# Kernel tuning notes

Measured on AMD Instinct MI355X. Metric: run time of the kernel, lower is better.

The kernel has to match this reference:

```python
import jax, jax.numpy as jnp
import numpy as np

H = 16  # heads
DH = 64  # dim_head
SCALE = DH ** -0.5


def rotate_half(x):
    x1, x2 = jnp.split(x, 2, axis=-1)
    return jnp.concatenate([-x2, x1], axis=-1)


def apply_rope(pos, t):
    # pos: [n, d] broadcast over [b, h, n, d]
    return t * jnp.cos(pos) + rotate_half(t) * jnp.sin(pos)


def setup_inputs() -> dict:
    key = jax.random.key(0)
    ks = jax.random.split(key, 6)
    B, N, D = 4, 2048, 1024
    inner = H * DH
    x = jax.random.normal(ks[0], (B, N, D), dtype=jnp.float32)
    rotary_emb = jax.random.normal(ks[1], (N, DH), dtype=jnp.float32)
    Wq = jax.random.normal(ks[2], (D, inner), dtype=jnp.float32) / np.sqrt(D)
    Wkv = jax.random.normal(ks[3], (D, 2 * inner), dtype=jnp.float32) / np.sqrt(D)
    Wout = jax.random.normal(ks[4], (inner, D), dtype=jnp.float32) / np.sqrt(inner)
    bout = jnp.zeros((D,), dtype=jnp.float32)
    return {"x": x, "rotary_emb": rotary_emb, "Wq": Wq, "Wkv": Wkv, "Wout": Wout, "bout": bout}


def reference(x, rotary_emb, Wq, Wkv, Wout, bout):
    B, N, D = x.shape
    # QKV projections (self-attention: context = x)
    q = x @ Wq                       # [b, n, h*d]
    kv = x @ Wkv                     # [b, n, 2*h*d]
    k, v = jnp.split(kv, 2, axis=-1)

    def to_heads(t):
        return t.reshape(B, N, H, DH).transpose(0, 2, 1, 3)  # [b, h, n, d]

    q, k, v = to_heads(q), to_heads(k), to_heads(v)
    q = apply_rope(rotary_emb, q)
    k = apply_rope(rotary_emb, k)

    # scaled dot-product attention
    scores = jnp.einsum('bhid,bhjd->bhij', q, k) * SCALE
    attn = jax.nn.softmax(scores, axis=-1)
    out = jnp.einsum('bhij,bhjd->bhid', attn, v)  # [b, h, n, d]
    out = out.transpose(0, 2, 1, 3).reshape(B, N, H * DH)
    return out @ Wout + bout
```

## Files before the change

### kernel.cpp

```cpp
#include <hip/hip_runtime.h>

#define BB 4
#define NN 2048
#define DD 1024
#define HH 16
#define DHH 64
#define MM (BB*NN)
#define QS 3072

typedef unsigned short u16;
typedef __attribute__((ext_vector_type(8))) short short8;
typedef __attribute__((ext_vector_type(4))) float floatx4;

#if __has_builtin(__builtin_amdgcn_exp2f)
#define EXP2F __builtin_amdgcn_exp2f
#else
#define EXP2F exp2f
#endif

__device__ __forceinline__ u16 f2bf(float f) {
  union { float f; unsigned u; } v; v.f = f;
  unsigned u = v.u;
  return (u16)((u + 0x7fffu + ((u >> 16) & 1u)) >> 16);
}
__device__ __forceinline__ float bf2f(u16 h) {
  union { unsigned u; float f; } v; v.u = ((unsigned)h) << 16;
  return v.f;
}
__device__ __forceinline__ unsigned fbits(float f) {
  union { float f; unsigned u; } v; v.f = f; return v.u;
}
__device__ __forceinline__ unsigned pkbf(float lo, float hi) {
#if __has_builtin(__builtin_amdgcn_perm)
  return __builtin_amdgcn_perm(fbits(hi), fbits(lo), 0x07060302u);
#else
  return (fbits(lo) >> 16) | (fbits(hi) & 0xffff0000u);
#endif
}
__device__ __forceinline__ void gll16(const u16* g, u16* l) {
  __builtin_amdgcn_global_load_lds((const __attribute__((address_space(1))) unsigned int*)g,
                                   (__attribute__((address_space(3))) unsigned int*)l, 16, 0, 0);
}
__device__ __forceinline__ int toff(int row, int kc) {
  int pr = row >> 1;
  int c = (((row & 1) << 2) + kc) ^ (pr & 7);
  return pr * 64 + c * 8;
}

#define SOFTMAX_SCALE 0.18033688f
#define SOFTMAX_BIAS  -28.8539008f

__global__ __launch_bounds__(256) void cvt_kernel(const float* __restrict__ in,
                                                  u16* __restrict__ out, int n) {
  int i = (blockIdx.x * 256 + threadIdx.x) * 4;
  if (i >= n) return;
  float4 v = *(const float4*)(in + i);
  u16 o[4] = {f2bf(v.x), f2bf(v.y), f2bf(v.z), f2bf(v.w)};
  *(uint2*)(out + i) = *(uint2*)o;
}

__global__ __launch_bounds__(256) void tcvt3_kernel(const float* __restrict__ Wq,
                                                    const float* __restrict__ Wkv,
                                                    const float* __restrict__ Wout,
                                                    u16* __restrict__ WT,
                                                    u16* __restrict__ WoutT) {
  __shared__ float t[64][65];
  int bx = blockIdx.x;
  const float* src;
  u16* dst;
  int C, c0;
  if (bx < 16)      { src = Wq;   dst = WT;                       C = 1024; c0 = bx * 64; }
  else if (bx < 48) { src = Wkv;  dst = WT + (size_t)DD * DD;     C = 2048; c0 = (bx - 16) * 64; }
  else              { src = Wout; dst = WoutT;                    C = 1024; c0 = (bx - 48) * 64; }
  const int R = 1024;
  int r0 = blockIdx.y * 64;
  int tid = threadIdx.x;
#pragma unroll
  for (int i = 0; i < 16; ++i) {
    int lin = i * 256 + tid;
    int rr = lin >> 6, cc = lin & 63;
    t[rr][cc] = src[(size_t)(r0 + rr) * C + c0 + cc];
  }
  __syncthreads();
#pragma unroll
  for (int i = 0; i < 16; ++i) {
    int lin = i * 256 + tid;
    int rr = lin >> 6, cc = lin & 63;
    dst[(size_t)(c0 + rr) * R + r0 + cc] = f2bf(t[cc][rr]);
  }
}

__global__ __launch_bounds__(256) void rope_tab_kernel(const float* __restrict__ rot,
                                                       float2* __restrict__ tab) {
  int i = blockIdx.x * 256 + threadIdx.x;
  float p = rot[i];
  float s, c;
  __sincosf(p, &s, &c);
  tab[i] = make_float2(c, s);
}

__global__ __launch_bounds__(512, 2) void gemm_qkv(const u16* __restrict__ A,
                                                   const u16* __restrict__ Bt,
                                                   u16* __restrict__ qd,
                                                   u16* __restrict__ kd,
                                                   u16* __restrict__ vt,
                                                   const float2* __restrict__ tab) {
  const int K = DD;
  const int NT = K / 64;
  __shared__ __align__(16) u16 lds[65536];
  int tid = threadIdx.x;
  int wave = tid >> 6, lane = tid & 63;
  int q4 = lane >> 4, l16 = lane & 15;
  int wr = wave >> 2, wc = wave & 3;

  int flat = blockIdx.y * 12 + blockIdx.x;
  int wg = (flat & 7) * 48 + (flat >> 3);
  int bx = wg % 12, by = wg / 12;
  int m0 = by * 256, n0 = bx * 256;

  const u16* Ag = A + (size_t)m0 * K;
  const u16* Bg = Bt + (size_t)n0 * K;

  int spr = tid >> 3, sct = tid & 7, su = sct ^ (spr & 7);
  int srow = spr * 2 + (su >> 2);
  int skc = (su & 3) * 8;
  size_t so = (size_t)srow * K + skc;

  int toffA[8], toffB[4];
#pragma unroll
  for (int mi = 0; mi < 8; ++mi) toffA[mi] = wr * 4096 + toff(mi * 16 + l16, q4);
#pragma unroll
  for (int ni = 0; ni < 4; ++ni)
    toffB[ni] = (wc >> 1) * 4096 + toff((wc & 1) * 64 + ni * 16 + l16, q4);

  floatx4 acc[8][4];
#pragma unroll
  for (int mi = 0; mi < 8; ++mi)
#pragma unroll
    for (int ni = 0; ni < 4; ++ni) acc[mi][ni] = (floatx4){0.f, 0.f, 0.f, 0.f};

  auto stageHalf = [&](int t, int mat, int kh) {
    const u16* src = (mat ? Bg : Ag) + so + t * 64 + kh * 32;
    u16* dst = lds + (t & 1) * 32768 + mat * 16384 + kh * 8192 + wave * 512;
    gll16(src, dst);
    gll16(src + (size_t)128 * K, dst + 4096);
  };

  stageHalf(0, 1, 0); stageHalf(0, 0, 0); stageHalf(0, 1, 1); stageHalf(0, 0, 1);
  stageHalf(1, 1, 0); stageHalf(1, 0, 0); stageHalf(1, 1, 1);
  __builtin_amdgcn_s_waitcnt(0x0F76);
  __builtin_amdgcn_s_barrier();

#pragma unroll
  for (int t = 0; t < NT; ++t) {
    const u16* Ab = lds + (t & 1) * 32768;
    const u16* Bb = Ab + 16384;
    short8 af[4], bfq[4];

#pragma unroll
    for (int ni = 0; ni < 4; ++ni) bfq[ni] = *(const short8*)(Bb + toffB[ni]);
#pragma unroll
    for (int f = 0; f < 4; ++f) af[f] = *(const short8*)(Ab + toffA[f]);
    if (t + 1 < NT) stageHalf(t + 1, 0, 1);
    __builtin_amdgcn_s_barrier();
    __builtin_amdgcn_s_waitcnt(0xC07F);
    __builtin_amdgcn_s_setprio(1);
#pragma unroll
    for (int f = 0; f < 4; ++f)
#pragma unroll
      for (int ni = 0; ni < 4; ++ni)
        acc[f][ni] = __builtin_amdgcn_mfma_f32_16x16x32_bf16(af[f], bfq[ni], acc[f][ni], 0, 0, 0);
    __builtin_amdgcn_s_setprio(0);
    __builtin_amdgcn_s_barrier();

#pragma unroll
    for (int f = 0; f < 4; ++f) af[f] = *(const short8*)(Ab + toffA[4 + f]);
    if (t + 2 < NT) stageHalf(t + 2, 1, 0);
    __builtin_amdgcn_s_barrier();
    __builtin_amdgcn_s_waitcnt(0xC07F);
    __builtin_amdgcn_s_setprio(1);
#pragma unroll
    for (int f = 0; f < 4; ++f)
#pragma unroll
      for (int ni = 0; ni < 4; ++ni)
        acc[4 + f][ni] = __builtin_amdgcn_mfma_f32_16x16x32_bf16(af[f], bfq[ni], acc[4 + f][ni], 0, 0, 0);
    __builtin_amdgcn_s_setprio(0);
    __builtin_amdgcn_s_barrier();

#pragma unroll
    for (int ni = 0; ni < 4; ++ni) bfq[ni] = *(const short8*)(Bb + 8192 + toffB[ni]);
#pragma unroll
    for (int f = 0; f < 4; ++f) af[f] = *(const short8*)(Ab + 8192 + toffA[f]);
    if (t + 2 < NT) stageHalf(t + 2, 0, 0);
    __builtin_amdgcn_s_barrier();
    __builtin_amdgcn_s_waitcnt(0xC07F);
    __builtin_amdgcn_s_setprio(1);
#pragma unroll
    for (int f = 0; f < 4; ++f)
#pragma unroll
      for (int ni = 0; ni < 4; ++ni)
        acc[f][ni] = __builtin_amdgcn_mfma_f32_16x16x32_bf16(af[f], bfq[ni], acc[f][ni], 0, 0, 0);
    __builtin_amdgcn_s_setprio(0);
    __builtin_amdgcn_s_barrier();

#pragma unroll
    for (int f = 0; f < 4; ++f) af[f] = *(const short8*)(Ab + 8192 + toffA[4 + f]);
    if (t + 2 < NT) stageHalf(t + 2, 1, 1);
    __builtin_amdgcn_s_barrier();
    __builtin_amdgcn_s_waitcnt(0xC07F);
    __builtin_amdgcn_s_setprio(1);
#pragma unroll
    for (int f = 0; f < 4; ++f)
#pragma unroll
      for (int ni = 0; ni < 4; ++ni)
        acc[4 + f][ni] = __builtin_amdgcn_mfma_f32_16x16x32_bf16(af[f], bfq[ni], acc[4 + f][ni], 0, 0, 0);
    __builtin_amdgcn_s_setprio(0);
    if (t == NT - 2) __builtin_amdgcn_s_waitcnt(0x0F70);
    else if (t < NT - 2) __builtin_amdgcn_s_waitcnt(0x0F76);
    __builtin_amdgcn_s_barrier();
  }

  int colbase = n0 + wc * 64;
  int slot = colbase >> 10;
  int h = (colbase >> 6) & 15;
#pragma unroll
  for (int mi = 0; mi < 8; ++mi) {
    int mbase = m0 + wr * 128 + mi * 16 + q4 * 4;
    float vals[4][4];
    if (slot < 2) {
      float scl = slot ? 1.0f : SOFTMAX_SCALE;
#pragma unroll
      for (int r = 0; r < 4; ++r) {
        int n = (mbase + r) & (NN - 1);
#pragma unroll
        for (int ni = 0; ni < 2; ++ni) {
          int d0 = ni * 16 + l16;
          float2 cs0 = tab[n * 64 + d0];
          float2 cs1 = tab[n * 64 + d0 + 32];
          float v0 = acc[mi][ni][r], v1 = acc[mi][ni + 2][r];
          vals[ni][r]     = (v0 * cs0.x - v1 * cs0.y) * scl;
          vals[ni + 2][r] = (v1 * cs1.x + v0 * cs1.y) * scl;
        }
      }
      u16* dst = slot ? kd : qd;
#pragma unroll
      for (int ni = 0; ni < 4; ++ni)
#pragma unroll
        for (int r = 0; r < 4; ++r) {
          int m = mbase + r;
          dst[((size_t)((m >> 11) * HH + h) * NN + (m & (NN - 1))) * 64 + ni * 16 + l16] =
              f2bf(vals[ni][r]);
        }
    } else {
#pragma unroll
      for (int ni = 0; ni < 4; ++ni) {
        int d = ni * 16 + l16;
#pragma unroll
        for (int r = 0; r < 4; ++r) {
          int m = mbase + r;
          int nn = m & (NN - 1);
          vt[(size_t)((m >> 11) * HH + h) * (NN * 64) + (nn >> 6) * 4096 + d * 64 + (nn & 63)] =
              f2bf(acc[mi][ni][r]);
        }
      }
    }
  }
}

__global__ __launch_bounds__(256) void gemm_out(const u16* __restrict__ A,
                                                const u16* __restrict__ Bt,
                                                float* __restrict__ Cout,
                                                const float* __restrict__ bias,
                                                int M, int N, int K) {
  __shared__ __align__(16) u16 lds[16384];
  int tid = threadIdx.x;
  int wave = tid >> 6, lane = tid & 63;
  int q4 = lane >> 4, l16 = lane & 15;
  int m0 = blockIdx.y * 128, n0 = blockIdx.x * 128;
  int wm = (wave >> 1) * 64, wn = (wave & 1) * 64;

  const u16* Ag = A + (size_t)m0 * K;
  const u16* Bg = Bt + (size_t)n0 * K;
  int o1 = tid, o2 = tid + 256;
  int pr1 = o1 >> 3, c1 = (o1 & 7) ^ (pr1 & 7);
  int row1 = pr1 * 2 + (c1 >> 2), kc1 = (c1 & 3) * 8;
  int pr2 = o2 >> 3, c2 = (o2 & 7) ^ (pr2 & 7);
  int row2 = pr2 * 2 + (c2 >> 2), kc2 = (c2 & 3) * 8;
  int d1 = wave * 512, d2 = 2048 + wave * 512;

  int foA[4], foB[4];
#pragma unroll
  for (int i = 0; i < 4; ++i) {
    foA[i] = toff(wm + i * 16 + l16, q4);
    foB[i] = toff(wn + i * 16 + l16, q4);
  }

  floatx4 acc[4][4];
#pragma unroll
  for (int mi = 0; mi < 4; ++mi)
#pragma unroll
    for (int ni = 0; ni < 4; ++ni) acc[mi][ni] = (floatx4){0.f, 0.f, 0.f, 0.f};

  gll16(Ag + (size_t)row1 * K + kc1, lds + d1);
  gll16(Ag + (size_t)row2 * K + kc2, lds + d2);
  gll16(Bg + (size_t)row1 * K + kc1, lds + 8192 + d1);
  gll16(Bg + (size_t)row2 * K + kc2, lds + 8192 + d2);

  for (int k0 = 0, it = 0; k0 < K; k0 += 32, ++it) {
    int boff = (it & 1) * 4096;
    if (k0 + 32 < K) {
      int nboff = 4096 - boff;
      int kn = k0 + 32;
      gll16(Ag + (size_t)row1 * K + kn + kc1, lds + nboff + d1);
      gll16(Ag + (size_t)row2 * K + kn + kc2, lds + nboff + d2);
      gll16(Bg + (size_t)row1 * K + kn + kc1, lds + 8192 + nboff + d1);
      gll16(Bg + (size_t)row2 * K + kn + kc2, lds + 8192 + nboff + d2);
      __builtin_amdgcn_s_waitcnt(0x0F74);
    } else {
      __builtin_amdgcn_s_waitcnt(0x0F70);
    }
    __builtin_amdgcn_s_barrier();
    const u16* Ac = lds + boff;
    const u16* Bc = lds + 8192 + boff;
    short8 af[4], bfr[4];
#pragma unroll
    for (int i = 0; i < 4; ++i) {
      af[i]  = *(const short8*)(Ac + foA[i]);
      bfr[i] = *(const short8*)(Bc + foB[i]);
    }
#pragma unroll
    for (int mi = 0; mi < 4; ++mi)
#pragma unroll
      for (int ni = 0; ni < 4; ++ni)
        acc[mi][ni] = __builtin_amdgcn_mfma_f32_16x16x32_bf16(af[mi], bfr[ni], acc[mi][ni], 0, 0, 0);
    __builtin_amdgcn_s_barrier();
  }

#pragma unroll
  for (int ni = 0; ni < 4; ++ni) {
    int col = n0 + wn + ni * 16 + l16;
    float bval = bias[col];
#pragma unroll
    for (int mi = 0; mi < 4; ++mi) {
#pragma unroll
      for (int r = 0; r < 4; ++r) {
        int row = m0 + wm + mi * 16 + q4 * 4 + r;
        Cout[(size_t)row * N + col] = acc[mi][ni][r] + bval;
      }
    }
  }
}

__global__ __launch_bounds__(512, 4) void attn_kernel(const u16* __restrict__ qd,
                                                      const u16* __restrict__ kd,
                                                      const u16* __restrict__ vt,
                                                      u16* __restrict__ ao) {
  __shared__ __align__(16) u16 lds[16384];

  int tid = threadIdx.x, wave = tid >> 6, lane = tid & 63;
  int q4 = lane >> 4, l16 = lane & 15;
  int qt = blockIdx.x, bh = blockIdx.y, b = bh >> 4, h = bh & 15;
  const u16* qbh = qd + (size_t)bh * NN * 64;
  const u16* kbh = kd + (size_t)bh * NN * 64;
  const u16* vbh = vt + (size_t)bh * NN * 64;

  int srow = wave * 8 + (lane >> 3);
  int g = ((lane & 7) ^ ((lane >> 3) & 7)) * 8;
  int prow = ((srow >> 2) & 3) * 8 + ((srow >> 4) & 1) * 4 + (srow & 3) + ((srow >> 5) & 1) * 32;

#pragma unroll
  for (int it = 0; it < 4; ++it)
    gll16(qbh + (size_t)(qt * 256 + it * 64 + srow) * 64 + g, lds + (it * 64 + wave * 8) * 64);
  __builtin_amdgcn_s_waitcnt(0x0F70);
  __builtin_amdgcn_s_barrier();

  short8 aq[2][2];
#pragma unroll
  for (int mi = 0; mi < 2; ++mi)
#pragma unroll
    for (int ks = 0; ks < 2; ++ks) {
      int row = wave * 32 + mi * 16 + l16;
      aq[mi][ks] = *(const short8*)(lds + row * 64 + (((ks * 4 + q4) ^ (row & 7)) * 8));
    }
  __builtin_amdgcn_s_waitcnt(0xC07F);
  __builtin_amdgcn_s_barrier();

  gll16(kbh + (size_t)prow * 64 + g, lds + wave * 512);
  gll16(vbh + (size_t)srow * 64 + g, lds + 8192 + wave * 512);

  union { unsigned u[4]; short8 s8; } ones;
#pragma unroll
  for (int i = 0; i < 4; ++i) ones.u[i] = 0x3F803F80u;

  floatx4 lacc[2];
  floatx4 o[2][4];
#pragma unroll
  for (int mi = 0; mi < 2; ++mi) {
    lacc[mi] = (floatx4){0.f, 0.f, 0.f, 0.f};
#pragma unroll
    for (int di = 0; di < 4; ++di) o[mi][di] = (floatx4){0.f, 0.f, 0.f, 0.f};
  }

  for (int j0 = 0, itn = 0; j0 < NN; j0 += 64, ++itn) {
    int coff = (itn & 1) * 4096;
    if (j0 + 64 < NN) {
      int noff = 4096 - coff;
      gll16(kbh + (size_t)(j0 + 64 + prow) * 64 + g, lds + noff + wave * 512);
      gll16(vbh + (size_t)((j0 >> 6) + 1) * 4096 + srow * 64 + g, lds + 8192 + noff + wave * 512);
      __builtin_amdgcn_s_waitcnt(0x0F72);
    } else {
      __builtin_amdgcn_s_waitcnt(0x0F70);
    }
    __builtin_amdgcn_s_barrier();

    const u16* Kc = lds + coff;
    const u16* Vc = lds + 8192 + coff;

    floatx4 s[4][2];
#pragma unroll
    for (int kg = 0; kg < 4; ++kg)
#pragma unroll
      for (int mi = 0; mi < 2; ++mi)
        s[kg][mi] = (floatx4){SOFTMAX_BIAS, SOFTMAX_BIAS, SOFTMAX_BIAS, SOFTMAX_BIAS};
#pragma unroll
    for (int ks = 0; ks < 2; ++ks) {
      short8 kf[4];
#pragma unroll
      for (int kg = 0; kg < 4; ++kg) {
        int row = kg * 16 + l16;
        kf[kg] = *(const short8*)(Kc + row * 64 + (((ks * 4 + q4) ^ (row & 7)) * 8));
      }
#pragma unroll
      for (int kg = 0; kg < 4; ++kg)
#pragma unroll
        for (int mi = 0; mi < 2; ++mi)
          s[kg][mi] = __builtin_amdgcn_mfma_f32_16x16x32_bf16(kf[kg], aq[mi][ks], s[kg][mi], 0, 0, 0);
    }

    unsigned pk[4][2][2];
#pragma unroll
    for (int kg = 0; kg < 4; ++kg)
#pragma unroll
      for (int mi = 0; mi < 2; ++mi) {
        float e0 = EXP2F(s[kg][mi][0]);
        float e1 = EXP2F(s[kg][mi][1]);
        float e2 = EXP2F(s[kg][mi][2]);
        float e3 = EXP2F(s[kg][mi][3]);
        pk[kg][mi][0] = pkbf(e0, e1);
        pk[kg][mi][1] = pkbf(e2, e3);
      }

#pragma unroll
    for (int ks = 0; ks < 2; ++ks) {
      short8 vf[4];
#pragma unroll
      for (int di = 0; di < 4; ++di) {
        int row = di * 16 + l16;
        vf[di] = *(const short8*)(Vc + row * 64 + (((ks * 4 + q4) ^ (row & 7)) * 8));
      }
#pragma unroll
      for (int mi = 0; mi < 2; ++mi) {
        union { unsigned u[4]; short8 s8; } bw;
        bw.u[0] = pk[2 * ks][mi][0];
        bw.u[1] = pk[2 * ks][mi][1];
        bw.u[2] = pk[2 * ks + 1][mi][0];
        bw.u[3] = pk[2 * ks + 1][mi][1];
        lacc[mi] = __builtin_amdgcn_mfma_f32_16x16x32_bf16(ones.s8, bw.s8, lacc[mi], 0, 0, 0);
#pragma unroll
        for (int di = 0; di < 4; ++di)
          o[mi][di] = __builtin_amdgcn_mfma_f32_16x16x32_bf16(vf[di], bw.s8, o[mi][di], 0, 0, 0);
      }
    }
    __builtin_amdgcn_s_barrier();
  }

  float rinv[2];
#pragma unroll
  for (int mi = 0; mi < 2; ++mi) rinv[mi] = 1.0f / lacc[mi][0];

#pragma unroll
  for (int mi = 0; mi < 2; ++mi) {
    int qrow = qt * 256 + wave * 32 + mi * 16 + l16;
    size_t base = (size_t)(b * NN + qrow) * DD + h * DHH + q4 * 4;
#pragma unroll
    for (int di = 0; di < 4; ++di)
#pragma unroll
      for (int r = 0; r < 4; ++r)
        ao[base + di * 16 + r] = f2bf(o[mi][di][r] * rinv[mi]);
  }
}

extern "C" void kernel_launch(void* const* d_in, const int* in_sizes, int n_in,
                              void* d_out, int out_size, void* d_ws, size_t ws_size,
                              hipStream_t stream) {
  const float* x    = (const float*)d_in[0];
  const float* rot  = (const float*)d_in[1];
  const float* Wq   = (const float*)d_in[2];
  const float* Wkv  = (const float*)d_in[3];
  const float* Wout = (const float*)d_in[4];
  const float* bout = (const float*)d_in[5];
  float* out = (float*)d_out;

  char* ws = (char*)d_ws;
  size_t off = 0;
  auto alloc = [&](size_t bytes) {
    void* p = ws + off;
    off = (off + bytes + 255) & ~(size_t)255;
    return p;
  };
  u16*    xb    = (u16*)alloc((size_t)MM * DD * 2);
  u16*    WT    = (u16*)alloc((size_t)QS * DD * 2);
  u16*    WoutT = (u16*)alloc((size_t)DD * DD * 2);
  float2* tab   = (float2*)alloc((size_t)NN * DHH * 8);
  u16*    qdb   = (u16*)alloc((size_t)MM * DD * 2);
  u16*    kdb   = (u16*)alloc((size_t)MM * DD * 2);
  u16*    vtt   = (u16*)alloc((size_t)MM * DD * 2);
  u16*    ao    = (u16*)alloc((size_t)MM * DD * 2);

  cvt_kernel<<<(MM * DD / 4) / 256, 256, 0, stream>>>(x, xb, MM * DD);
  tcvt3_kernel<<<dim3(64, 16), 256, 0, stream>>>(Wq, Wkv, Wout, WT, WoutT);
  rope_tab_kernel<<<(NN * DHH) / 256, 256, 0, stream>>>(rot, tab);

  gemm_qkv<<<dim3(QS / 256, MM / 256), 512, 0, stream>>>(xb, WT, qdb, kdb, vtt, tab);

  attn_kernel<<<dim3(NN / 256, BB * HH), 512, 0, stream>>>(qdb, kdb, vtt, ao);

  gemm_out<<<dim3(DD / 128, MM / 128), 256, 0, stream>>>(ao, WoutT, out, bout, MM, DD, DD);
}
```

Measured before the change: 269.1 us.

## Double-buffer MFMA register fragments to overlap LDS reads with compute

The GEMM main loop now holds two sets of A/B register fragments, so the LDS reads for the next MFMA phase are issued before the current phase's MFMAs run. Partial lgkmcnt waits let computation start while those reads are still in flight. The global-load waitcnt is moved to before the barrier in the third phase, and sched_barriers stop the compiler from reordering across phases. The cost is higher VGPR pressure and more delicate waitcnt correctness.

```diff
diff --git a/kernel.cpp b/kernel.cpp
--- a/kernel.cpp
+++ b/kernel.cpp
@@ -150,73 +150,87 @@
   stageHalf(1, 1, 0); stageHalf(1, 0, 0); stageHalf(1, 1, 1);
   __builtin_amdgcn_s_waitcnt(0x0F76);
   __builtin_amdgcn_s_barrier();
+  __builtin_amdgcn_sched_barrier(0);
+
+  short8 af0[4], af1[4], bfq0[4], bfq1[4];
+#pragma unroll
+  for (int ni = 0; ni < 4; ++ni) bfq0[ni] = *(const short8*)(lds + 16384 + toffB[ni]);
+#pragma unroll
+  for (int f = 0; f < 4; ++f) af0[f] = *(const short8*)(lds + toffA[f]);
 
 #pragma unroll
   for (int t = 0; t < NT; ++t) {
     const u16* Ab = lds + (t & 1) * 32768;
     const u16* Bb = Ab + 16384;
-    short8 af[4], bfq[4];
-
-#pragma unroll
-    for (int ni = 0; ni < 4; ++ni) bfq[ni] = *(const short8*)(Bb + toffB[ni]);
-#pragma unroll
-    for (int f = 0; f < 4; ++f) af[f] = *(const short8*)(Ab + toffA[f]);
+    const u16* Abn = lds + ((t + 1) & 1) * 32768;
+    const u16* Bbn = Abn + 16384;
+
+#pragma unroll
+    for (int f = 0; f < 4; ++f) af1[f] = *(const short8*)(Ab + toffA[4 + f]);
     if (t + 1 < NT) stageHalf(t + 1, 0, 1);
     __builtin_amdgcn_s_barrier();
-    __builtin_amdgcn_s_waitcnt(0xC07F);
+    __builtin_amdgcn_sched_barrier(0);
+    __builtin_amdgcn_s_waitcnt(0xC47F);
     __builtin_amdgcn_s_setprio(1);
 #pragma unroll
     for (int f = 0; f < 4; ++f)
 #pragma unroll
       for (int ni = 0; ni < 4; ++ni)
-        acc[f][ni] = __builtin_amdgcn_mfma_f32_16x16x32_bf16(af[f], bfq[ni], acc[f][ni], 0, 0, 0);
+        acc[f][ni] = __builtin_amdgcn_mfma_f32_16x16x32_bf16(af0[f], bfq0[ni], acc[f][ni], 0, 0, 0);
     __builtin_amdgcn_s_setprio(0);
     __builtin_amdgcn_s_barrier();
 
 #pragma unroll
-    for (int f = 0; f < 4; ++f) af[f] = *(const short8*)(Ab + toffA[4 + f]);
+    for (int ni = 0; ni < 4; ++ni) bfq1[ni] = *(const short8*)(Bb + 8192 + toffB[ni]);
+#pragma unroll
+    for (int f = 0; f < 4; ++f) af0[f] = *(const short8*)(Ab + 8192 + toffA[f]);
     if (t + 2 < NT) stageHalf(t + 2, 1, 0);
     __builtin_amdgcn_s_barrier();
-    __builtin_amdgcn_s_waitcnt(0xC07F);
+    __builtin_amdgcn_sched_barrier(0);
+    __builtin_amdgcn_s_waitcnt(0xC87F);
     __builtin_amdgcn_s_setprio(1);
 #pragma unroll
     for (int f = 0; f < 4; ++f)
 #pragma unroll
       for (int ni = 0; ni < 4; ++ni)
-        acc[4 + f][ni] = __builtin_amdgcn_mfma_f32_16x16x32_bf16(af[f], bfq[ni], acc[4 + f][ni], 0, 0, 0);
+        acc[4 + f][ni] = __builtin_amdgcn_mfma_f32_16x16x32_bf16(af1[f], bfq0[ni], acc[4 + f][ni], 0, 0, 0);
     __builtin_amdgcn_s_setprio(0);
     __builtin_amdgcn_s_barrier();
 
 #pragma unroll
-    for (int ni = 0; ni < 4; ++ni) bfq[ni] = *(const short8*)(Bb + 8192 + toffB[ni]);
-#pragma unroll
-    for (int f = 0; f < 4; ++f) af[f] = *(const short8*)(Ab + 8192 + toffA[f]);
+    for (int f = 0; f < 4; ++f) af1[f] = *(const short8*)(Ab + 8192 + toffA[4 + f]);
     if (t + 2 < NT) stageHalf(t + 2, 0, 0);
-    __builtin_amdgcn_s_barrier();
-    __builtin_amdgcn_s_waitcnt(0xC07F);
+    if (t < NT - 2) __builtin_amdgcn_s_waitcnt(0x0F74);
+    else if (t == NT - 2) __builtin_amdgcn_s_waitcnt(0x0F70);
+    __builtin_amdgcn_s_barrier();
+    __builtin_amdgcn_sched_barrier(0);
+    __builtin_amdgcn_s_waitcnt(0xC47F);
     __builtin_amdgcn_s_setprio(1);
 #pragma unroll
     for (int f = 0; f < 4; ++f)
 #pragma unroll
       for (int ni = 0; ni < 4; ++ni)
-        acc[f][ni] = __builtin_amdgcn_mfma_f32_16x16x32_bf16(af[f], bfq[ni], acc[f][ni], 0, 0, 0);
+        acc[f][ni] = __builtin_amdgcn_mfma_f32_16x16x32_bf16(af0[f], bfq1[ni], acc[f][ni], 0, 0, 0);
     __builtin_amdgcn_s_setprio(0);
     __builtin_amdgcn_s_barrier();
 
-#pragma unroll
-    for (int f = 0; f < 4; ++f) af[f] = *(const short8*)(Ab + 8192 + toffA[4 + f]);
+    if (t + 1 < NT) {
+#pragma unroll
+      for (int ni = 0; ni < 4; ++ni) bfq0[ni] = *(const short8*)(Bbn + toffB[ni]);
+#pragma unroll
+      for (int f = 0; f < 4; ++f) af0[f] = *(const short8*)(Abn + toffA[f]);
+    }
     if (t + 2 < NT) stageHalf(t + 2, 1, 1);
     __builtin_amdgcn_s_barrier();
-    __builtin_amdgcn_s_waitcnt(0xC07F);
+    __builtin_amdgcn_sched_barrier(0);
+    __builtin_amdgcn_s_waitcnt(0xC87F);
     __builtin_amdgcn_s_setprio(1);
 #pragma unroll
     for (int f = 0; f < 4; ++f)
 #pragma unroll
       for (int ni = 0; ni < 4; ++ni)
-        acc[4 + f][ni] = __builtin_amdgcn_mfma_f32_16x16x32_bf16(af[f], bfq[ni], acc[4 + f][ni], 0, 0, 0);
+        acc[4 + f][ni] = __builtin_amdgcn_mfma_f32_16x16x32_bf16(af1[f], bfq1[ni], acc[4 + f][ni], 0, 0, 0);
     __builtin_amdgcn_s_setprio(0);
-    if (t == NT - 2) __builtin_amdgcn_s_waitcnt(0x0F70);
-    else if (t < NT - 2) __builtin_amdgcn_s_waitcnt(0x0F76);
     __builtin_amdgcn_s_barrier();
   }
 
```

Result: faster. 259.1 us (-3.7%).

## Split QKV GEMM into QK and V kernels with vectorized epilogue stores

Applied to the files above, without the earlier changes.

The fused QKV projection is split into a 256x256-tile kernel for Q and K and a separate 128x128-tile kernel for V. In the QK kernel the MFMA operand order is swapped so that each lane holds four consecutive head-dim values, which lets the RoPE epilogue write packed 8-byte stores instead of scattered 2-byte stores. The V kernel also writes its transposed layout with packed stores. The cost is an extra kernel launch, a smaller and less efficient GEMM tile for V, and x being read again by the second kernel.

```diff
diff --git a/kernel.cpp b/kernel.cpp
--- a/kernel.cpp
+++ b/kernel.cpp
@@ -99,12 +99,11 @@
   tab[i] = make_float2(c, s);
 }
 
-__global__ __launch_bounds__(512, 2) void gemm_qkv(const u16* __restrict__ A,
-                                                   const u16* __restrict__ Bt,
-                                                   u16* __restrict__ qd,
-                                                   u16* __restrict__ kd,
-                                                   u16* __restrict__ vt,
-                                                   const float2* __restrict__ tab) {
+__global__ __launch_bounds__(512, 2) void gemm_qk(const u16* __restrict__ A,
+                                                  const u16* __restrict__ Bt,
+                                                  u16* __restrict__ qd,
+                                                  u16* __restrict__ kd,
+                                                  const float2* __restrict__ tab) {
   const int K = DD;
   const int NT = K / 64;
   __shared__ __align__(16) u16 lds[65536];
@@ -113,9 +112,9 @@
   int q4 = lane >> 4, l16 = lane & 15;
   int wr = wave >> 2, wc = wave & 3;
 
-  int flat = blockIdx.y * 12 + blockIdx.x;
-  int wg = (flat & 7) * 48 + (flat >> 3);
-  int bx = wg % 12, by = wg / 12;
+  int flat = blockIdx.y * 8 + blockIdx.x;
+  int wg = (flat & 7) * 32 + (flat >> 3);
+  int bx = wg & 7, by = wg >> 3;
   int m0 = by * 256, n0 = bx * 256;
 
   const u16* Ag = A + (size_t)m0 * K;
@@ -169,7 +168,7 @@
     for (int f = 0; f < 4; ++f)
 #pragma unroll
       for (int ni = 0; ni < 4; ++ni)
-        acc[f][ni] = __builtin_amdgcn_mfma_f32_16x16x32_bf16(af[f], bfq[ni], acc[f][ni], 0, 0, 0);
+        acc[f][ni] = __builtin_amdgcn_mfma_f32_16x16x32_bf16(bfq[ni], af[f], acc[f][ni], 0, 0, 0);
     __builtin_amdgcn_s_setprio(0);
     __builtin_amdgcn_s_barrier();
 
@@ -183,7 +182,7 @@
     for (int f = 0; f < 4; ++f)
 #pragma unroll
       for (int ni = 0; ni < 4; ++ni)
-        acc[4 + f][ni] = __builtin_amdgcn_mfma_f32_16x16x32_bf16(af[f], bfq[ni], acc[4 + f][ni], 0, 0, 0);
+        acc[4 + f][ni] = __builtin_amdgcn_mfma_f32_16x16x32_bf16(bfq[ni], af[f], acc[4 + f][ni], 0, 0, 0);
     __builtin_amdgcn_s_setprio(0);
     __builtin_amdgcn_s_barrier();
 
@@ -199,7 +198,7 @@
     for (int f = 0; f < 4; ++f)
 #pragma unroll
       for (int ni = 0; ni < 4; ++ni)
-        acc[f][ni] = __builtin_amdgcn_mfma_f32_16x16x32_bf16(af[f], bfq[ni], acc[f][ni], 0, 0, 0);
+        acc[f][ni] = __builtin_amdgcn_mfma_f32_16x16x32_bf16(bfq[ni], af[f], acc[f][ni], 0, 0, 0);
     __builtin_amdgcn_s_setprio(0);
     __builtin_amdgcn_s_barrier();
 
@@ -213,56 +212,128 @@
     for (int f = 0; f < 4; ++f)
 #pragma unroll
       for (int ni = 0; ni < 4; ++ni)
-        acc[4 + f][ni] = __builtin_amdgcn_mfma_f32_16x16x32_bf16(af[f], bfq[ni], acc[4 + f][ni], 0, 0, 0);
+        acc[4 + f][ni] = __builtin_amdgcn_mfma_f32_16x16x32_bf16(bfq[ni], af[f], acc[4 + f][ni], 0, 0, 0);
     __builtin_amdgcn_s_setprio(0);
     if (t == NT - 2) __builtin_amdgcn_s_waitcnt(0x0F70);
     else if (t < NT - 2) __builtin_amdgcn_s_waitcnt(0x0F76);
     __builtin_amdgcn_s_barrier();
   }
 
-  int colbase = n0 + wc * 64;
-  int slot = colbase >> 10;
-  int h = (colbase >> 6) & 15;
+  int h = (n0 + wc * 64) >> 6;
+  u16* dst = (h < 16) ? qd : kd;
+  int hh = h & 15;
+  float scl = (h < 16) ? SOFTMAX_SCALE : 1.0f;
+  int b = m0 >> 11;
+  int tokbase = (m0 & (NN - 1)) + wr * 128;
 #pragma unroll
   for (int mi = 0; mi < 8; ++mi) {
-    int mbase = m0 + wr * 128 + mi * 16 + q4 * 4;
-    float vals[4][4];
-    if (slot < 2) {
-      float scl = slot ? 1.0f : SOFTMAX_SCALE;
+    int tok = tokbase + mi * 16 + l16;
+    u16* rowp = dst + ((size_t)(b * HH + hh) * NN + tok) * 64;
+    const float2* tb = tab + tok * 64;
+#pragma unroll
+    for (int ni = 0; ni < 2; ++ni) {
+      int d0 = ni * 16 + q4 * 4;
+      u16 plo[4], phi[4];
 #pragma unroll
       for (int r = 0; r < 4; ++r) {
-        int n = (mbase + r) & (NN - 1);
-#pragma unroll
-        for (int ni = 0; ni < 2; ++ni) {
-          int d0 = ni * 16 + l16;
-          float2 cs0 = tab[n * 64 + d0];
-          float2 cs1 = tab[n * 64 + d0 + 32];
-          float v0 = acc[mi][ni][r], v1 = acc[mi][ni + 2][r];
-          vals[ni][r]     = (v0 * cs0.x - v1 * cs0.y) * scl;
-          vals[ni + 2][r] = (v1 * cs1.x + v0 * cs1.y) * scl;
-        }
+        float2 cs0 = tb[d0 + r];
+        float2 cs1 = tb[d0 + r + 32];
+        float v0 = acc[mi][ni][r], v1 = acc[mi][ni + 2][r];
+        plo[r] = f2bf((v0 * cs0.x - v1 * cs0.y) * scl);
+        phi[r] = f2bf((v1 * cs1.x + v0 * cs1.y) * scl);
       }
-      u16* dst = slot ? kd : qd;
+      *(uint2*)(rowp + d0) = *(uint2*)plo;
+      *(uint2*)(rowp + d0 + 32) = *(uint2*)phi;
+    }
+  }
+}
+
+__global__ __launch_bounds__(256) void gemm_v(const u16* __restrict__ A,
+                                              const u16* __restrict__ Bt,
+                                              u16* __restrict__ vt) {
+  const int K = DD;
+  __shared__ __align__(16) u16 lds[16384];
+  int tid = threadIdx.x;
+  int wave = tid >> 6, lane = tid & 63;
+  int q4 = lane >> 4, l16 = lane & 15;
+
+  int flat = blockIdx.y * 8 + blockIdx.x;
+  int wg = (flat & 7) * 64 + (flat >> 3);
+  int bx = wg & 7, by = wg >> 3;
+  int m0 = by * 128, n0 = bx * 128;
+
+  int wm = (wave >> 1) * 64, wn = (wave & 1) * 64;
+
+  const u16* Ag = A + (size_t)m0 * K;
+  const u16* Bg = Bt + (size_t)(2048 + n0) * K;
+  int o1 = tid, o2 = tid + 256;
+  int pr1 = o1 >> 3, c1 = (o1 & 7) ^ (pr1 & 7);
+  int row1 = pr1 * 2 + (c1 >> 2), kc1 = (c1 & 3) * 8;
+  int pr2 = o2 >> 3, c2 = (o2 & 7) ^ (pr2 & 7);
+  int row2 = pr2 * 2 + (c2 >> 2), kc2 = (c2 & 3) * 8;
+  int d1 = wave * 512, d2 = 2048 + wave * 512;
+
+  int foA[4], foB[4];
+#pragma unroll
+  for (int i = 0; i < 4; ++i) {
+    foA[i] = toff(wm + i * 16 + l16, q4);
+    foB[i] = toff(wn + i * 16 + l16, q4);
+  }
+
+  floatx4 acc[4][4];
+#pragma unroll
+  for (int mi = 0; mi < 4; ++mi)
+#pragma unroll
+    for (int ni = 0; ni < 4; ++ni) acc[mi][ni] = (floatx4){0.f, 0.f, 0.f, 0.f};
+
+  gll16(Ag + (size_t)row1 * K + kc1, lds + d1);
+  gll16(Ag + (size_t)row2 * K + kc2, lds + d2);
+  gll16(Bg + (size_t)row1 * K + kc1, lds + 8192 + d1);
+  gll16(Bg + (size_t)row2 * K + kc2, lds + 8192 + d2);
+
+  for (int k0 = 0, it = 0; k0 < K; k0 += 32, ++it) {
+    int boff = (it & 1) * 4096;
+    if (k0 + 32 < K) {
+      int nboff = 4096 - boff;
+      int kn = k0 + 32;
+      gll16(Ag + (size_t)row1 * K + kn + kc1, lds + nboff + d1);
+      gll16(Ag + (size_t)row2 * K + kn + kc2, lds + nboff + d2);
+      gll16(Bg + (size_t)row1 * K + kn + kc1, lds + 8192 + nboff + d1);
+      gll16(Bg + (size_t)row2 * K + kn + kc2, lds + 8192 + nboff + d2);
+      __builtin_amdgcn_s_waitcnt(0x0F74);
+    } else {
+      __builtin_amdgcn_s_waitcnt(0x0F70);
+    }
+    __builtin_amdgcn_s_barrier();
+    const u16* Ac = lds + boff;
+    const u16* Bc = lds + 8192 + boff;
+    short8 af[4], bfr[4];
+#pragma unroll
+    for (int i = 0; i < 4; ++i) {
+      af[i]  = *(const short8*)(Ac + foA[i]);
+      bfr[i] = *(const short8*)(Bc + foB[i]);
+    }
+#pragma unroll
+    for (int mi = 0; mi < 4; ++mi)
 #pragma unroll
       for (int ni = 0; ni < 4; ++ni)
-#pragma unroll
-        for (int r = 0; r < 4; ++r) {
-          int m = mbase + r;
-          dst[((size_t)((m >> 11) * HH + h) * NN + (m & (NN - 1))) * 64 + ni * 16 + l16] =
-              f2bf(vals[ni][r]);
-        }
-    } else {
-#pragma unroll
-      for (int ni = 0; ni < 4; ++ni) {
-        int d = ni * 16 + l16;
-#pragma unroll
-        for (int r = 0; r < 4; ++r) {
-          int m = mbase + r;
-          int nn = m & (NN - 1);
-          vt[(size_t)((m >> 11) * HH + h) * (NN * 64) + (nn >> 6) * 4096 + d * 64 + (nn & 63)] =
-              f2bf(acc[mi][ni][r]);
-        }
-      }
+        acc[mi][ni] = __builtin_amdgcn_mfma_f32_16x16x32_bf16(af[mi], bfr[ni], acc[mi][ni], 0, 0, 0);
+    __builtin_amdgcn_s_barrier();
+  }
+
+  int h = (n0 + wn) >> 6;
+#pragma unroll
+  for (int mi = 0; mi < 4; ++mi) {
+    int mbase = m0 + wm + mi * 16 + q4 * 4;
+    int b = mbase >> 11;
+    int nn = mbase & (NN - 1);
+    u16* base = vt + (size_t)(b * HH + h) * (NN * 64) + (nn >> 6) * 4096 + (nn & 63);
+#pragma unroll
+    for (int ni = 0; ni < 4; ++ni) {
+      int d = ni * 16 + l16;
+      u16 p[4] = {f2bf(acc[mi][ni][0]), f2bf(acc[mi][ni][1]),
+                  f2bf(acc[mi][ni][2]), f2bf(acc[mi][ni][3])};
+      *(uint2*)(base + d * 64) = *(uint2*)p;
     }
   }
 }
@@ -521,7 +592,8 @@
   tcvt3_kernel<<<dim3(64, 16), 256, 0, stream>>>(Wq, Wkv, Wout, WT, WoutT);
   rope_tab_kernel<<<(NN * DHH) / 256, 256, 0, stream>>>(rot, tab);
 
-  gemm_qkv<<<dim3(QS / 256, MM / 256), 512, 0, stream>>>(xb, WT, qdb, kdb, vtt, tab);
+  gemm_qk<<<dim3(8, 32), 512, 0, stream>>>(xb, WT, qdb, kdb, tab);
+  gemm_v<<<dim3(8, 64), 256, 0, stream>>>(xb, WT, vtt);
 
   attn_kernel<<<dim3(NN / 256, BB * HH), 512, 0, stream>>>(qdb, kdb, vtt, ao);
 
```

New measurement: 270.6 us. Within noise of the previous version (+0.6%).
